# Kernel optimization log

Hardware: AMD Instinct MI355X
Metric: run time of the kernel (lower is better)

Reference implementation:

```python
import jax, jax.numpy as jnp
import numpy as np


def _norm(graph):
    # graph: [B, N, N]. Row-normalize: D^{-1} A, with nan/inf -> 0.
    degree = jnp.sum(graph, axis=2)            # [B, N]
    inv = 1.0 / degree
    inv = jnp.where(jnp.isnan(inv) | jnp.isinf(inv), jnp.zeros_like(inv), inv)
    # diag_embed(inv) @ graph == inv[:, :, None] * graph (per-row scale)
    return inv[:, :, None] * graph


def setup_inputs() -> dict:
    key = jax.random.key(0)
    k0, k1 = jax.random.split(key)
    B, N = 16, 1024
    adj0 = jax.random.uniform(k0, (B, N, N), dtype=jnp.float32)
    adj1 = jax.random.uniform(k1, (B, N, N), dtype=jnp.float32)
    return {"adj0": adj0, "adj1": adj1}


def reference(adj0, adj1):
    return (_norm(adj0), _norm(adj1))
```

## Files before the change

kernel.cpp:

```cpp
#include <hip/hip_runtime.h>

#define NCOLS 1024

__global__ __launch_bounds__(256) void Normalizer_row_kernel(
    const float* __restrict__ a0, const float* __restrict__ a1,
    float* __restrict__ out, int rows_per_input) {
    int row = blockIdx.x;
    const float* src;
    float* dst;
    if (row < rows_per_input) {
        src = a0 + (size_t)row * NCOLS;
        dst = out + (size_t)row * NCOLS;
    } else {
        int r = row - rows_per_input;
        src = a1 + (size_t)r * NCOLS;
        dst = out + (size_t)rows_per_input * NCOLS + (size_t)r * NCOLS;
    }

    const int tid = threadIdx.x;
    float4 v = reinterpret_cast<const float4*>(src)[tid];

    float s = (v.x + v.y) + (v.z + v.w);
#pragma unroll
    for (int off = 32; off > 0; off >>= 1)
        s += __shfl_down(s, off, 64);

    __shared__ float ws[4];
    const int lane = tid & 63;
    const int wave = tid >> 6;
    if (lane == 0) ws[wave] = s;
    __syncthreads();

    float deg = (ws[0] + ws[1]) + (ws[2] + ws[3]);
    float inv = 1.0f / deg;
    if (!isfinite(inv)) inv = 0.0f;

    float4 o;
    o.x = v.x * inv;
    o.y = v.y * inv;
    o.z = v.z * inv;
    o.w = v.w * inv;
    reinterpret_cast<float4*>(dst)[tid] = o;
}

extern "C" void kernel_launch(void* const* d_in, const int* in_sizes, int n_in,
                              void* d_out, int out_size, void* d_ws, size_t ws_size,
                              hipStream_t stream) {
    const float* a0 = (const float*)d_in[0];
    const float* a1 = (const float*)d_in[1];
    float* out = (float*)d_out;

    const int rows_per_input = in_sizes[0] / NCOLS;
    const int total_rows = 2 * rows_per_input;

    Normalizer_row_kernel<<<total_rows, 256, 0, stream>>>(a0, a1, out, rows_per_input);
}
```

Before: 220.9 us.

## Map one row per wavefront with nontemporal vector loads and stores

Each 64-lane wavefront now normalizes a whole row, so the degree reduction needs only wave shuffles and the shared-memory write plus block barrier are gone. Blocks cover four rows each, cutting the grid size by four. Loads and stores switch to nontemporal builtins so streaming data is not kept in cache. This assumes the total row count is a multiple of four and that every row has exactly 1024 columns.

```diff
diff --git a/kernel.cpp b/kernel.cpp
--- a/kernel.cpp
+++ b/kernel.cpp
@@ -2,45 +2,47 @@
 
 #define NCOLS 1024
 
+typedef float vfloat4 __attribute__((ext_vector_type(4)));
+
 __global__ __launch_bounds__(256) void Normalizer_row_kernel(
     const float* __restrict__ a0, const float* __restrict__ a1,
     float* __restrict__ out, int rows_per_input) {
-    int row = blockIdx.x;
-    const float* src;
-    float* dst;
-    if (row < rows_per_input) {
-        src = a0 + (size_t)row * NCOLS;
-        dst = out + (size_t)row * NCOLS;
-    } else {
-        int r = row - rows_per_input;
-        src = a1 + (size_t)r * NCOLS;
-        dst = out + (size_t)rows_per_input * NCOLS + (size_t)r * NCOLS;
-    }
+    const int tid  = threadIdx.x;
+    const int lane = tid & 63;
+    const int wave = tid >> 6;
+    const int row  = blockIdx.x * 4 + wave;
 
-    const int tid = threadIdx.x;
-    float4 v = reinterpret_cast<const float4*>(src)[tid];
+    const float* src = (row < rows_per_input)
+        ? a0 + (size_t)row * NCOLS
+        : a1 + (size_t)(row - rows_per_input) * NCOLS;
+    float* dst = out + (size_t)row * NCOLS;
 
-    float s = (v.x + v.y) + (v.z + v.w);
+    const vfloat4* src4 = reinterpret_cast<const vfloat4*>(src);
+    vfloat4* dst4 = reinterpret_cast<vfloat4*>(dst);
+
+    vfloat4 v0 = __builtin_nontemporal_load(&src4[lane]);
+    vfloat4 v1 = __builtin_nontemporal_load(&src4[lane + 64]);
+    vfloat4 v2 = __builtin_nontemporal_load(&src4[lane + 128]);
+    vfloat4 v3 = __builtin_nontemporal_load(&src4[lane + 192]);
+
+    float s = ((v0.x + v0.y) + (v0.z + v0.w)) + ((v1.x + v1.y) + (v1.z + v1.w))
+            + ((v2.x + v2.y) + (v2.z + v2.w)) + ((v3.x + v3.y) + (v3.z + v3.w));
 #pragma unroll
     for (int off = 32; off > 0; off >>= 1)
-        s += __shfl_down(s, off, 64);
+        s += __shfl_xor(s, off, 64);
 
-    __shared__ float ws[4];
-    const int lane = tid & 63;
-    const int wave = tid >> 6;
-    if (lane == 0) ws[wave] = s;
-    __syncthreads();
-
-    float deg = (ws[0] + ws[1]) + (ws[2] + ws[3]);
-    float inv = 1.0f / deg;
+    float inv = 1.0f / s;
     if (!isfinite(inv)) inv = 0.0f;
 
-    float4 o;
-    o.x = v.x * inv;
-    o.y = v.y * inv;
-    o.z = v.z * inv;
-    o.w = v.w * inv;
-    reinterpret_cast<float4*>(dst)[tid] = o;
+    v0 *= inv;
+    v1 *= inv;
+    v2 *= inv;
+    v3 *= inv;
+
+    __builtin_nontemporal_store(v0, &dst4[lane]);
+    __builtin_nontemporal_store(v1, &dst4[lane + 64]);
+    __builtin_nontemporal_store(v2, &dst4[lane + 128]);
+    __builtin_nontemporal_store(v3, &dst4[lane + 192]);
 }
 
 extern "C" void kernel_launch(void* const* d_in, const int* in_sizes, int n_in,
@@ -52,6 +54,7 @@
 
     const int rows_per_input = in_sizes[0] / NCOLS;
     const int total_rows = 2 * rows_per_input;
+    const int blocks = total_rows / 4;
 
-    Normalizer_row_kernel<<<total_rows, 256, 0, stream>>>(a0, a1, out, rows_per_input);
+    Normalizer_row_kernel<<<blocks, 256, 0, stream>>>(a0, a1, out, rows_per_input);
 }
```

Result: no change. 219.1 us (-0.8%).
